# Optimization experiments

Measured on AMD Instinct MI355X. Metric: run time of the kernel, lower is better.

Reference implementation:

```python
import jax, jax.numpy as jnp
import numpy as np

N_INP = 128
N_HID = 512
N_OUT = 256
N_HEADS = 64
N_SM = 4
EPS_GN = 1e-5
TINY = 1e-14


def setup_inputs() -> dict:
    key = jax.random.key(0)
    ks = jax.random.split(key, 8)
    s = 0.05  # small init scale keeps softplus/softmax in a sane range
    f32 = jnp.float32
    return {
        "x": jax.random.normal(ks[0], (N_INP, N_INP), f32),
        "last_out_sm": jax.random.uniform(ks[1], (N_OUT, N_HEADS), f32),
        # grouped-conv weights, stored per-head with conv singleton dims squeezed
        "qw": jax.random.normal(ks[2], (N_HEADS, N_INP), f32) * s,            # Conv2d q
        "w1": jax.random.normal(ks[3], (N_HEADS, N_HID, N_INP), f32) * s,     # Conv1d l1
        "gn1_g": jnp.ones((N_HEADS, N_HID), f32),                             # GroupNorm ln_l1
        "gn1_b": jnp.zeros((N_HEADS, N_HID), f32),
        "w2": jax.random.normal(ks[4], (N_SM, N_HEADS, N_OUT, N_HID), f32) * s,  # Conv1d l2_n
        "gn2_g": jnp.ones((N_SM, N_HEADS, N_OUT), f32),                       # GroupNorm ln_l2_n
        "gn2_b": jnp.zeros((N_SM, N_HEADS, N_OUT), f32),
        "ws": jax.random.normal(ks[5], (N_HEADS, N_OUT, N_OUT), f32) * s,     # Conv1d scalar
        "woo": jax.random.normal(ks[6], (N_HEADS, 2 * N_OUT), f32) * s,       # Conv1d on_off
    }


def _group_norm(z, g, b):
    # normalize over the last (per-head channel) axis, biased variance, then affine
    mu = z.mean(-1, keepdims=True)
    var = z.var(-1, keepdims=True)
    return (z - mu) * jax.lax.rsqrt(var + EPS_GN) * g + b


def reference(x, last_out_sm, qw, w1, gn1_g, gn1_b, w2, gn2_g, gn2_b, ws, woo):
    n_out = last_out_sm.shape[0]
    # q: grouped Conv2d with kernel (1, n_inp) on replicated x -> per-head x @ qw_h
    sub = jnp.einsum("rc,hc->hr", x, qw)                     # (H, n_inp)
    # l1 (grouped 1x1 conv == per-head matmul) + GroupNorm(n_heads groups) + softplus
    h1 = jax.nn.softplus(_group_norm(jnp.einsum("hoi,hi->ho", w1, sub), gn1_g, gn1_b))  # (H, n_hid)
    # l2_n branches: per-head matmul + GroupNorm + softmax over n_out, summed over n_sm
    z = _group_norm(jnp.einsum("shoi,hi->sho", w2, h1), gn2_g, gn2_b)  # (S, H, n_out)
    out_sm = jax.nn.softmax(z, axis=-1).sum(0).T             # (n_out, H)
    # scalar branch: grouped 1x1 conv applied to ones -> row-sum of per-head weight
    scalar = ws.sum(-1).T                                    # (n_out, H)
    # on_off gate: per-head dot of [prod(last_out_sm, dim1), out_sm[:, h]] with woo_h
    last_prod = jnp.prod(last_out_sm, axis=1)                # (n_out,)
    gate_logit = woo[:, :n_out] @ last_prod + jnp.einsum("ho,oh->h", woo[:, n_out:], out_sm)
    on_off = jax.nn.sigmoid(gate_logit)                      # (H,)
    on_off_out_sm = on_off[None, :] * out_sm                 # (n_out, H)
    out_scaled = on_off_out_sm * scalar
    out_scaled = jnp.where(jnp.abs(out_scaled) <= TINY, TINY, out_scaled)
    return (jnp.clip(on_off_out_sm, TINY, None), out_scaled)
```

## Files before the change

kernel.cpp:

```cpp
#include <hip/hip_runtime.h>
#include <math.h>

#define N_INP 128
#define N_HID 512
#define N_OUT 256
#define N_HEADS 64
#define N_SM 4
#define EPS_GN 1e-5f
#define TINY 1e-14f

__device__ __forceinline__ float wave_sum(float v) {
#pragma unroll
  for (int off = 32; off; off >>= 1) v += __shfl_down(v, off);
  return v;
}
__device__ __forceinline__ float wave_max(float v) {
#pragma unroll
  for (int off = 32; off; off >>= 1) v = fmaxf(v, __shfl_down(v, off));
  return v;
}

__device__ __forceinline__ float block_sum(float v, float* red) {
  int wave = threadIdx.x >> 6, lane = threadIdx.x & 63;
  int nw = blockDim.x >> 6;
  v = wave_sum(v);
  __syncthreads();
  if (lane == 0) red[wave] = v;
  __syncthreads();
  float s = 0.f;
  for (int i = 0; i < nw; ++i) s += red[i];
  return s;
}
__device__ __forceinline__ float block_max(float v, float* red) {
  int wave = threadIdx.x >> 6, lane = threadIdx.x & 63;
  int nw = blockDim.x >> 6;
  v = wave_max(v);
  __syncthreads();
  if (lane == 0) red[wave] = v;
  __syncthreads();
  float s = -3.4e38f;
  for (int i = 0; i < nw; ++i) s = fmaxf(s, red[i]);
  return s;
}
__device__ __forceinline__ float2 block_sum2(float a, float b, float2* red2) {
  int wave = threadIdx.x >> 6, lane = threadIdx.x & 63;
  int nw = blockDim.x >> 6;
#pragma unroll
  for (int off = 32; off; off >>= 1) {
    a += __shfl_down(a, off);
    b += __shfl_down(b, off);
  }
  __syncthreads();
  if (lane == 0) red2[wave] = make_float2(a, b);
  __syncthreads();
  float2 s = make_float2(0.f, 0.f);
  for (int i = 0; i < nw; ++i) { s.x += red2[i].x; s.y += red2[i].y; }
  return s;
}

__global__ __launch_bounds__(512) void k_z1(
    const float* __restrict__ x, const float* __restrict__ qw,
    const float* __restrict__ w1, float* __restrict__ z1,
    float* __restrict__ osm) {
  int blk = blockIdx.x;
  int h = blk >> 2, oq = blk & 3;
  int tid = threadIdx.x, wave = tid >> 6, lane = tid & 63;
  __shared__ float sub_s[N_INP];

  if (tid < 64) osm[blk * 64 + tid] = 0.f;

  float2 qv = ((const float2*)(qw + h * N_INP))[lane];
  for (int r = wave; r < N_INP; r += 8) {
    float2 xv = ((const float2*)(x + r * N_INP))[lane];
    float p = wave_sum(xv.x * qv.x + xv.y * qv.y);
    if (lane == 0) sub_s[r] = p;
  }
  __syncthreads();

  float2 sv = ((const float2*)sub_s)[lane];
  const float* w1h = w1 + ((size_t)h * N_HID + (size_t)oq * 128) * N_INP;
  for (int k = 0; k < 16; ++k) {
    int o = wave * 16 + k;
    float2 wv = ((const float2*)(w1h + (size_t)o * N_INP))[lane];
    float p = wave_sum(wv.x * sv.x + wv.y * sv.y);
    if (lane == 0) z1[h * N_HID + oq * 128 + o] = p;
  }
}

__global__ __launch_bounds__(1024) void k_l2_scalar(
    const float* __restrict__ z1, const float* __restrict__ g1,
    const float* __restrict__ b1, const float* __restrict__ w2,
    const float* __restrict__ g2, const float* __restrict__ b2,
    const float* __restrict__ wsc, float* __restrict__ osm,
    float* __restrict__ scal) {
  int blk = blockIdx.x;
  int s = blk >> 6, h = blk & 63;
  int tid = threadIdx.x, wave = tid >> 6, lane = tid & 63;
  __shared__ float h1_s[N_HID];
  __shared__ float z_s[N_OUT];
  __shared__ float2 red2[16];
  __shared__ float red[16];

  const float* w2base = w2 + (size_t)blk * N_OUT * N_HID;
  const float4* row0 = (const float4*)(w2base + (size_t)(wave * 16) * N_HID);
  float4 wa = row0[lane];
  float4 wb = row0[64 + lane];

  float v1 = (tid < N_HID) ? z1[h * N_HID + tid] : 0.f;
  float2 s1 = block_sum2(v1, v1 * v1, red2);
  float mu1 = s1.x * (1.f / N_HID);
  float var1 = s1.y * (1.f / N_HID) - mu1 * mu1;
  float r1 = rsqrtf(var1 + EPS_GN);
  if (tid < N_HID) {
    float zz = (v1 - mu1) * r1 * g1[h * N_HID + tid] + b1[h * N_HID + tid];
    h1_s[tid] = fmaxf(zz, 0.f) + log1pf(expf(-fabsf(zz)));
  }
  __syncthreads();

  float4 ha = ((const float4*)h1_s)[lane];
  float4 hb = ((const float4*)h1_s)[64 + lane];

  for (int k = 0; k < 4; ++k) {
    int o = s * 64 + wave * 4 + k;
    float4 v = ((const float4*)(wsc + ((size_t)(h * N_OUT + o)) * N_OUT))[lane];
    float p = wave_sum(v.x + v.y + v.z + v.w);
    if (lane == 0) scal[o * N_HEADS + h] = p;
  }

  for (int k = 0; k < 16; ++k) {
    float4 na, nb;
    if (k < 15) {
      const float4* row = (const float4*)(w2base + (size_t)(wave * 16 + k + 1) * N_HID);
      na = row[lane];
      nb = row[64 + lane];
    }
    float p = wa.x * ha.x + wa.y * ha.y + wa.z * ha.z + wa.w * ha.w +
              wb.x * hb.x + wb.y * hb.y + wb.z * hb.z + wb.w * hb.w;
    p = wave_sum(p);
    if (lane == 0) z_s[wave * 16 + k] = p;
    wa = na; wb = nb;
  }
  __syncthreads();

  float v = (tid < N_OUT) ? z_s[tid] : 0.f;
  float2 sz = block_sum2(v, v * v, red2);
  float mu = sz.x * (1.f / N_OUT);
  float var = sz.y * (1.f / N_OUT) - mu * mu;
  float rs = rsqrtf(var + EPS_GN);
  float zn = (tid < N_OUT)
                 ? (v - mu) * rs * g2[(size_t)blk * N_OUT + tid] + b2[(size_t)blk * N_OUT + tid]
                 : -3.4e38f;
  float mx = block_max(zn, red);
  float e = (tid < N_OUT) ? expf(zn - mx) : 0.f;
  float es = block_sum(e, red);
  if (tid < N_OUT) atomicAdd(&osm[tid * N_HEADS + h], e / es);
}

__global__ __launch_bounds__(256) void k_gate_final(
    const float* __restrict__ last, const float* __restrict__ woo,
    const float* __restrict__ osm, const float* __restrict__ scal,
    float* __restrict__ out) {
  int h = blockIdx.x;
  int tid = threadIdx.x;
  __shared__ float red[4];

  const float4* row = (const float4*)(last + (size_t)tid * N_HEADS);
  float p = 1.f;
#pragma unroll
  for (int j = 0; j < 16; ++j) {
    float4 v = row[j];
    p *= v.x * v.y * v.z * v.w;
  }
  float o_sm = osm[tid * N_HEADS + h];
  float part = woo[h * 2 * N_OUT + tid] * p +
               woo[h * 2 * N_OUT + N_OUT + tid] * o_sm;
  float logit = block_sum(part, red);
  float oo = 1.f / (1.f + expf(-logit));

  float v0 = oo * o_sm;
  out[tid * N_HEADS + h] = fmaxf(v0, TINY);
  float v1 = v0 * scal[tid * N_HEADS + h];
  out[N_OUT * N_HEADS + tid * N_HEADS + h] = (fabsf(v1) <= TINY) ? TINY : v1;
}

extern "C" void kernel_launch(void* const* d_in, const int* in_sizes, int n_in,
                              void* d_out, int out_size, void* d_ws, size_t ws_size,
                              hipStream_t stream) {
  const float* x    = (const float*)d_in[0];
  const float* last = (const float*)d_in[1];
  const float* qw   = (const float*)d_in[2];
  const float* w1   = (const float*)d_in[3];
  const float* g1   = (const float*)d_in[4];
  const float* b1   = (const float*)d_in[5];
  const float* w2   = (const float*)d_in[6];
  const float* g2   = (const float*)d_in[7];
  const float* b2   = (const float*)d_in[8];
  const float* wsc  = (const float*)d_in[9];
  const float* woo  = (const float*)d_in[10];
  float* out = (float*)d_out;
  float* ws  = (float*)d_ws;

  float* z1   = ws;
  float* osm  = ws + 32768;
  float* scal = ws + 49152;

  hipLaunchKernelGGL(k_z1,        dim3(256), dim3(512),  0, stream, x, qw, w1, z1, osm);
  hipLaunchKernelGGL(k_l2_scalar, dim3(256), dim3(1024), 0, stream, z1, g1, b1, w2, g2, b2, wsc, osm, scal);
  hipLaunchKernelGGL(k_gate_final,dim3(64),  dim3(256),  0, stream, last, woo, osm, scal, out);
}
```

Baseline: 261.6 us.

## Fuse gate kernel into l2 kernel via last-block counter and precompute GN1 stats

```diff
diff --git a/kernel.cpp b/kernel.cpp
--- a/kernel.cpp
+++ b/kernel.cpp
@@ -42,32 +42,18 @@
   for (int i = 0; i < nw; ++i) s = fmaxf(s, red[i]);
   return s;
 }
-__device__ __forceinline__ float2 block_sum2(float a, float b, float2* red2) {
-  int wave = threadIdx.x >> 6, lane = threadIdx.x & 63;
-  int nw = blockDim.x >> 6;
-#pragma unroll
-  for (int off = 32; off; off >>= 1) {
-    a += __shfl_down(a, off);
-    b += __shfl_down(b, off);
-  }
-  __syncthreads();
-  if (lane == 0) red2[wave] = make_float2(a, b);
-  __syncthreads();
-  float2 s = make_float2(0.f, 0.f);
-  for (int i = 0; i < nw; ++i) { s.x += red2[i].x; s.y += red2[i].y; }
-  return s;
-}
 
 __global__ __launch_bounds__(512) void k_z1(
     const float* __restrict__ x, const float* __restrict__ qw,
     const float* __restrict__ w1, float* __restrict__ z1,
-    float* __restrict__ osm) {
+    float* __restrict__ zstat, int* __restrict__ cnt) {
   int blk = blockIdx.x;
   int h = blk >> 2, oq = blk & 3;
   int tid = threadIdx.x, wave = tid >> 6, lane = tid & 63;
   __shared__ float sub_s[N_INP];
-
-  if (tid < 64) osm[blk * 64 + tid] = 0.f;
+  __shared__ float2 wred[8];
+
+  if (blk == 0 && tid < N_HEADS) cnt[tid] = 0;
 
   float2 qv = ((const float2*)(qw + h * N_INP))[lane];
   for (int r = wave; r < N_INP; r += 8) {
@@ -79,20 +65,31 @@
 
   float2 sv = ((const float2*)sub_s)[lane];
   const float* w1h = w1 + ((size_t)h * N_HID + (size_t)oq * 128) * N_INP;
+  float zs = 0.f, zq = 0.f;
   for (int k = 0; k < 16; ++k) {
     int o = wave * 16 + k;
     float2 wv = ((const float2*)(w1h + (size_t)o * N_INP))[lane];
     float p = wave_sum(wv.x * sv.x + wv.y * sv.y);
-    if (lane == 0) z1[h * N_HID + oq * 128 + o] = p;
-  }
-}
-
-__global__ __launch_bounds__(1024) void k_l2_scalar(
-    const float* __restrict__ z1, const float* __restrict__ g1,
-    const float* __restrict__ b1, const float* __restrict__ w2,
-    const float* __restrict__ g2, const float* __restrict__ b2,
-    const float* __restrict__ wsc, float* __restrict__ osm,
-    float* __restrict__ scal) {
+    if (lane == 0) { z1[h * N_HID + oq * 128 + o] = p; zs += p; zq += p * p; }
+  }
+  if (lane == 0) wred[wave] = make_float2(zs, zq);
+  __syncthreads();
+  if (tid == 0) {
+    float a = 0.f, b = 0.f;
+    for (int i = 0; i < 8; ++i) { a += wred[i].x; b += wred[i].y; }
+    zstat[blk * 2] = a;
+    zstat[blk * 2 + 1] = b;
+  }
+}
+
+__global__ __launch_bounds__(1024) void k_l2_gate(
+    const float* __restrict__ z1, const float* __restrict__ zstat,
+    const float* __restrict__ g1, const float* __restrict__ b1,
+    const float* __restrict__ w2, const float* __restrict__ g2,
+    const float* __restrict__ b2, const float* __restrict__ wsc,
+    const float* __restrict__ last, const float* __restrict__ woo,
+    float* __restrict__ part, float* __restrict__ scal,
+    int* __restrict__ cnt, float* __restrict__ out) {
   int blk = blockIdx.x;
   int s = blk >> 6, h = blk & 63;
   int tid = threadIdx.x, wave = tid >> 6, lane = tid & 63;
@@ -100,18 +97,24 @@
   __shared__ float z_s[N_OUT];
   __shared__ float2 red2[16];
   __shared__ float red[16];
+  __shared__ int done_s;
 
   const float* w2base = w2 + (size_t)blk * N_OUT * N_HID;
   const float4* row0 = (const float4*)(w2base + (size_t)(wave * 16) * N_HID);
   float4 wa = row0[lane];
   float4 wb = row0[64 + lane];
 
-  float v1 = (tid < N_HID) ? z1[h * N_HID + tid] : 0.f;
-  float2 s1 = block_sum2(v1, v1 * v1, red2);
-  float mu1 = s1.x * (1.f / N_HID);
-  float var1 = s1.y * (1.f / N_HID) - mu1 * mu1;
+  float zsum = 0.f, zsq = 0.f;
+#pragma unroll
+  for (int q = 0; q < 4; ++q) {
+    zsum += zstat[(h * 4 + q) * 2];
+    zsq  += zstat[(h * 4 + q) * 2 + 1];
+  }
+  float mu1 = zsum * (1.f / N_HID);
+  float var1 = zsq * (1.f / N_HID) - mu1 * mu1;
   float r1 = rsqrtf(var1 + EPS_GN);
   if (tid < N_HID) {
+    float v1 = z1[h * N_HID + tid];
     float zz = (v1 - mu1) * r1 * g1[h * N_HID + tid] + b1[h * N_HID + tid];
     h1_s[tid] = fmaxf(zz, 0.f) + log1pf(expf(-fabsf(zz)));
   }
@@ -127,6 +130,7 @@
     if (lane == 0) scal[o * N_HEADS + h] = p;
   }
 
+  float as = 0.f, aq = 0.f;
   for (int k = 0; k < 16; ++k) {
     float4 na, nb;
     if (k < 15) {
@@ -137,50 +141,54 @@
     float p = wa.x * ha.x + wa.y * ha.y + wa.z * ha.z + wa.w * ha.w +
               wb.x * hb.x + wb.y * hb.y + wb.z * hb.z + wb.w * hb.w;
     p = wave_sum(p);
-    if (lane == 0) z_s[wave * 16 + k] = p;
+    if (lane == 0) { z_s[wave * 16 + k] = p; as += p; aq += p * p; }
     wa = na; wb = nb;
   }
-  __syncthreads();
-
-  float v = (tid < N_OUT) ? z_s[tid] : 0.f;
-  float2 sz = block_sum2(v, v * v, red2);
+  if (lane == 0) red2[wave] = make_float2(as, aq);
+  __syncthreads();
+
+  float2 sz = make_float2(0.f, 0.f);
+  for (int i = 0; i < 16; ++i) { sz.x += red2[i].x; sz.y += red2[i].y; }
   float mu = sz.x * (1.f / N_OUT);
   float var = sz.y * (1.f / N_OUT) - mu * mu;
   float rs = rsqrtf(var + EPS_GN);
   float zn = (tid < N_OUT)
-                 ? (v - mu) * rs * g2[(size_t)blk * N_OUT + tid] + b2[(size_t)blk * N_OUT + tid]
+                 ? (z_s[tid] - mu) * rs * g2[(size_t)blk * N_OUT + tid] + b2[(size_t)blk * N_OUT + tid]
                  : -3.4e38f;
   float mx = block_max(zn, red);
   float e = (tid < N_OUT) ? expf(zn - mx) : 0.f;
   float es = block_sum(e, red);
-  if (tid < N_OUT) atomicAdd(&osm[tid * N_HEADS + h], e / es);
-}
-
-__global__ __launch_bounds__(256) void k_gate_final(
-    const float* __restrict__ last, const float* __restrict__ woo,
-    const float* __restrict__ osm, const float* __restrict__ scal,
-    float* __restrict__ out) {
-  int h = blockIdx.x;
-  int tid = threadIdx.x;
-  __shared__ float red[4];
-
-  const float4* row = (const float4*)(last + (size_t)tid * N_HEADS);
-  float p = 1.f;
-#pragma unroll
-  for (int j = 0; j < 16; ++j) {
-    float4 v = row[j];
-    p *= v.x * v.y * v.z * v.w;
-  }
-  float o_sm = osm[tid * N_HEADS + h];
-  float part = woo[h * 2 * N_OUT + tid] * p +
-               woo[h * 2 * N_OUT + N_OUT + tid] * o_sm;
-  float logit = block_sum(part, red);
-  float oo = 1.f / (1.f + expf(-logit));
-
-  float v0 = oo * o_sm;
-  out[tid * N_HEADS + h] = fmaxf(v0, TINY);
-  float v1 = v0 * scal[tid * N_HEADS + h];
-  out[N_OUT * N_HEADS + tid * N_HEADS + h] = (fabsf(v1) <= TINY) ? TINY : v1;
+  if (tid < N_OUT) part[(size_t)blk * N_OUT + tid] = e / es;
+
+  __threadfence();
+  if (tid == 0) done_s = atomicAdd(&cnt[h], 1);
+  __syncthreads();
+  if (done_s == 3) {
+    __threadfence();
+    float gpart = 0.f, osum = 0.f;
+    if (tid < N_OUT) {
+      int o = tid;
+#pragma unroll
+      for (int ss = 0; ss < 4; ++ss)
+        osum += part[(size_t)(ss * 64 + h) * N_OUT + o];
+      const float4* rowL = (const float4*)(last + (size_t)o * N_HEADS);
+      float lp = 1.f;
+#pragma unroll
+      for (int j = 0; j < 16; ++j) {
+        float4 v = rowL[j];
+        lp *= v.x * v.y * v.z * v.w;
+      }
+      gpart = woo[h * 2 * N_OUT + o] * lp + woo[h * 2 * N_OUT + N_OUT + o] * osum;
+    }
+    float logit = block_sum(gpart, red);
+    float oo = 1.f / (1.f + expf(-logit));
+    if (tid < N_OUT) {
+      float v0 = oo * osum;
+      out[tid * N_HEADS + h] = fmaxf(v0, TINY);
+      float v1 = v0 * scal[tid * N_HEADS + h];
+      out[N_OUT * N_HEADS + tid * N_HEADS + h] = (fabsf(v1) <= TINY) ? TINY : v1;
+    }
+  }
 }
 
 extern "C" void kernel_launch(void* const* d_in, const int* in_sizes, int n_in,
@@ -200,11 +208,15 @@
   float* out = (float*)d_out;
   float* ws  = (float*)d_ws;
 
-  float* z1   = ws;
-  float* osm  = ws + 32768;
-  float* scal = ws + 49152;
-
-  hipLaunchKernelGGL(k_z1,        dim3(256), dim3(512),  0, stream, x, qw, w1, z1, osm);
-  hipLaunchKernelGGL(k_l2_scalar, dim3(256), dim3(1024), 0, stream, z1, g1, b1, w2, g2, b2, wsc, osm, scal);
-  hipLaunchKernelGGL(k_gate_final,dim3(64),  dim3(256),  0, stream, last, woo, osm, scal, out);
-}
+  float* z1    = ws;
+  float* zstat = ws + 32768;
+  float* part  = ws + 33280;
+  float* scal  = ws + 98816;
+  int*   cnt   = (int*)(ws + 115200);
+
+  hipLaunchKernelGGL(k_z1,      dim3(256), dim3(512),  0, stream,
+                     x, qw, w1, z1, zstat, cnt);
+  hipLaunchKernelGGL(k_l2_gate, dim3(256), dim3(1024), 0, stream,
+                     z1, zstat, g1, b1, w2, g2, b2, wsc, last, woo,
+                     part, scal, cnt, out);
+}
```

Result: slower. 329.6 us (+26.0%).
